# Optimization experiments

Measured on AMD Instinct MI355X. Metric: run time of the kernel, lower is better.

The kernel has to match this reference:

```python
import jax, jax.numpy as jnp
import numpy as np

DIM = 192
HEADS = 6
G = 16          # window size (ds_flag=0 dense attention)
B = 1
H_SZ = 256
W_SZ = 256
POS_DIM = 12    # (dim//4)//4
HIDDEN = 768    # 4*dim


def _ln(x, g, b, eps=1e-5):
    m = jnp.mean(x, -1, keepdims=True)
    v = jnp.var(x, -1, keepdims=True)
    return (x - m) / jnp.sqrt(v + eps) * g + b


def setup_inputs() -> dict:
    key = jax.random.key(0)
    ks = jax.random.split(key, 8)
    s = 0.05
    return {
        "x": jax.random.normal(ks[0], (B, H_SZ * W_SZ, DIM), jnp.float32),
        "gamma1": jnp.ones((DIM,), jnp.float32),
        "beta1": jnp.zeros((DIM,), jnp.float32),
        "qkv_w": jax.random.normal(ks[1], (DIM, 3 * DIM), jnp.float32) * s,
        "qkv_b": jnp.zeros((3 * DIM,), jnp.float32),
        "proj_w": jax.random.normal(ks[2], (DIM, DIM), jnp.float32) * s,
        "proj_b": jnp.zeros((DIM,), jnp.float32),
        "pos_proj_w": jax.random.normal(ks[3], (2, POS_DIM), jnp.float32) * s,
        "pos_proj_b": jnp.zeros((POS_DIM,), jnp.float32),
        "ln1_g": jnp.ones((POS_DIM,), jnp.float32),
        "ln1_b": jnp.zeros((POS_DIM,), jnp.float32),
        "pos1_w": jax.random.normal(ks[4], (POS_DIM, POS_DIM), jnp.float32) * s,
        "pos1_b": jnp.zeros((POS_DIM,), jnp.float32),
        "ln2_g": jnp.ones((POS_DIM,), jnp.float32),
        "ln2_b": jnp.zeros((POS_DIM,), jnp.float32),
        "pos2_w": jax.random.normal(ks[5], (POS_DIM, POS_DIM), jnp.float32) * s,
        "pos2_b": jnp.zeros((POS_DIM,), jnp.float32),
        "ln3_g": jnp.ones((POS_DIM,), jnp.float32),
        "ln3_b": jnp.zeros((POS_DIM,), jnp.float32),
        "pos3_w": jax.random.normal(ks[6], (POS_DIM, HEADS), jnp.float32) * s,
        "pos3_b": jnp.zeros((HEADS,), jnp.float32),
        "gamma2": jnp.ones((DIM,), jnp.float32),
        "beta2": jnp.zeros((DIM,), jnp.float32),
        "fc1_w": jax.random.normal(ks[7], (DIM, HIDDEN), jnp.float32) * s,
        "fc1_b": jnp.zeros((HIDDEN,), jnp.float32),
        "fc2_w": jax.random.normal(jax.random.fold_in(key, 9), (HIDDEN, DIM), jnp.float32) * s,
        "fc2_b": jnp.zeros((DIM,), jnp.float32),
        "H": H_SZ,
        "W": W_SZ,
    }


def reference(x, gamma1, beta1, qkv_w, qkv_b, proj_w, proj_b,
              pos_proj_w, pos_proj_b, ln1_g, ln1_b, pos1_w, pos1_b,
              ln2_g, ln2_b, pos2_w, pos2_b, ln3_g, ln3_b, pos3_w, pos3_b,
              gamma2, beta2, fc1_w, fc1_b, fc2_w, fc2_b, H, W):
    Bx, L, C = x.shape
    h = HEADS
    d = C // h
    N = G * G
    shortcut = x
    xn = _ln(x, gamma1, beta1)
    # window partition (H, W divisible by G -> no padding, attn_mask=None)
    xw = xn.reshape(Bx, H // G, G, W // G, G, C).transpose(0, 1, 3, 2, 4, 5)
    xw = xw.reshape(-1, N, C)                       # [B_, N, C]
    B_ = xw.shape[0]
    qkv = (xw @ qkv_w + qkv_b).reshape(B_, N, 3, h, d)
    q = qkv[:, :, 0].transpose(0, 2, 1, 3) * (d ** -0.5)   # [B_, h, N, d]
    k = qkv[:, :, 1].transpose(0, 2, 1, 3)
    v = qkv[:, :, 2].transpose(0, 2, 1, 3)
    attn = jnp.einsum('bhnd,bhmd->bhnm', q, k)      # [B_, h, N, N]
    # dynamic relative position bias (DynamicPosBias MLP + gather)
    r = jnp.arange(1 - G, G)
    biases = jnp.stack(jnp.meshgrid(r, r, indexing='ij')).reshape(2, -1).T.astype(x.dtype)  # [(2G-1)^2, 2]
    p = biases @ pos_proj_w + pos_proj_b
    p = jax.nn.relu(_ln(p, ln1_g, ln1_b)) @ pos1_w + pos1_b
    p = jax.nn.relu(_ln(p, ln2_g, ln2_b)) @ pos2_w + pos2_b
    p = jax.nn.relu(_ln(p, ln3_g, ln3_b)) @ pos3_w + pos3_b  # [(2G-1)^2, heads]
    c = jnp.stack(jnp.meshgrid(jnp.arange(G), jnp.arange(G), indexing='ij')).reshape(2, -1)
    rel = c[:, :, None] - c[:, None, :]             # [2, N, N]
    idx = (rel[0] + G - 1) * (2 * G - 1) + (rel[1] + G - 1)  # [N, N]
    attn = attn + p[idx].transpose(2, 0, 1)[None]   # add [1, h, N, N] bias
    attn = jax.nn.softmax(attn, axis=-1)
    out = jnp.einsum('bhnm,bhmd->bhnd', attn, v).transpose(0, 2, 1, 3).reshape(B_, N, C)
    out = out @ proj_w + proj_b
    # window reverse
    out = out.reshape(Bx, H // G, W // G, G, G, C).transpose(0, 1, 3, 2, 4, 5).reshape(Bx, L, C)
    x = shortcut + out
    y = _ln(x, gamma2, beta2)
    y = jax.nn.gelu(y @ fc1_w + fc1_b, approximate=False) @ fc2_w + fc2_b
    return x + y
```

## Files before the change

### kernel.cpp

```cpp
#include <hip/hip_runtime.h>
#include <hip/hip_bf16.h>

#define DIM 192
#define HEADS 6
#define QKV_N 576
#define HIDDEN 768
#define M_ROWS 65536

typedef unsigned short ushortT;
typedef __attribute__((ext_vector_type(8))) short short8v;
typedef __attribute__((ext_vector_type(4))) float f32x4;
typedef __attribute__((ext_vector_type(4))) unsigned int u32x4;

#define QSCALE_L2E 0.2550348649f
#define LOG2E 1.4426950408889634f

__device__ __forceinline__ float bf2f(ushortT u) {
    union { unsigned int i; float f; } c; c.i = ((unsigned int)u) << 16; return c.f;
}
__device__ __forceinline__ ushortT f2bf(float f) {
    union { float f; unsigned int i; } c; c.f = f;
    unsigned int i = c.i;
    return (ushortT)((i + 0x7fffu + ((i >> 16) & 1u)) >> 16);
}
__device__ __forceinline__ float fast_gelu(float v) {
    float x3 = v * v * v;
    float z = fmaf(x3, -0.1029537917f, v * -2.302205077f);
    float e = exp2f(z);
    return v * __builtin_amdgcn_rcpf(1.0f + e);
}

#define GLOBAL_LOAD_LDS16(gp, lp) \
    __builtin_amdgcn_global_load_lds((const __attribute__((address_space(1))) void*)(gp), \
                                     (__attribute__((address_space(3))) void*)(lp), 16, 0, 0)

__device__ __forceinline__ void ln_relu_mm12(const float* in, const float* g, const float* b,
                                             const float* w, const float* bb, float* out, int nout) {
    float m = 0.f;
#pragma unroll
    for (int j = 0; j < 12; ++j) m += in[j];
    m *= (1.0f / 12.0f);
    float v = 0.f;
#pragma unroll
    for (int j = 0; j < 12; ++j) { float d = in[j] - m; v += d * d; }
    v *= (1.0f / 12.0f);
    float r = rsqrtf(v + 1e-5f);
    float t[12];
#pragma unroll
    for (int j = 0; j < 12; ++j) t[j] = fmaxf((in[j] - m) * r * g[j] + b[j], 0.0f);
    for (int j2 = 0; j2 < nout; ++j2) {
        float s = bb[j2];
#pragma unroll
        for (int j = 0; j < 12; ++j) s = fmaf(t[j], w[j * nout + j2], s);
        out[j2] = s;
    }
}

__global__ __launch_bounds__(256) void prep_kernel(
        const float* __restrict__ qkv_w, const float* __restrict__ proj_w,
        const float* __restrict__ fc1_w, const float* __restrict__ fc2_w,
        ushortT* __restrict__ qkv_wt, ushortT* __restrict__ proj_wt,
        ushortT* __restrict__ fc1_wt, ushortT* __restrict__ fc2_wt,
        const float* __restrict__ pw, const float* __restrict__ pb,
        const float* __restrict__ g1, const float* __restrict__ b1,
        const float* __restrict__ w1, const float* __restrict__ bb1,
        const float* __restrict__ g2, const float* __restrict__ b2,
        const float* __restrict__ w2, const float* __restrict__ bb2,
        const float* __restrict__ g3, const float* __restrict__ b3,
        const float* __restrict__ w3, const float* __restrict__ bb3,
        float* __restrict__ BTf) {
    __shared__ float tile[32][33];
    int blk = blockIdx.x;
    int t = threadIdx.x;
    if (blk < 432) {
        const float* W; ushortT* Wt; int K, N, bx, by; bool perm = false;
        if (blk < 108)      { W = qkv_w;  Wt = qkv_wt;  K = 192; N = 576; bx = blk % 18;        by = blk / 18; }
        else if (blk < 144) { int r = blk - 108; W = proj_w; Wt = proj_wt; K = 192; N = 192; bx = r % 6;  by = r / 6; }
        else if (blk < 288) { int r = blk - 144; W = fc1_w;  Wt = fc1_wt;  K = 192; N = 768; bx = r % 24; by = r / 24; }
        else                { int r = blk - 288; W = fc2_w;  Wt = fc2_wt;  K = 768; N = 192; bx = r % 6;  by = r / 6; perm = true; }
        int tx = t & 31, ty = t >> 5;
        int bX = bx * 32, bY = by * 32;
#pragma unroll
        for (int i = 0; i < 32; i += 8)
            tile[ty + i][tx] = W[(size_t)(bY + ty + i) * N + bX + tx];
        __syncthreads();
        int kcol = perm ? (((tx & 15) << 1) | (tx >> 4)) : tx;
#pragma unroll
        for (int i = 0; i < 32; i += 8)
            Wt[(size_t)(bX + ty + i) * K + bY + kcol] = f2bf(tile[tx][ty + i]);
    } else {
        int blk2 = blk - 432;
        int h = blk2 >> 8, q = blk2 & 255, kv = t;
        float di = (float)((q >> 4) - (kv >> 4));
        float dj = (float)((q & 15) - (kv & 15));
        float a[12], hh[12];
#pragma unroll
        for (int j = 0; j < 12; ++j) a[j] = di * pw[j] + dj * pw[12 + j] + pb[j];
        ln_relu_mm12(a, g1, b1, w1, bb1, hh, 12);
        ln_relu_mm12(hh, g2, b2, w2, bb2, a, 12);
        float m = 0.f;
#pragma unroll
        for (int j = 0; j < 12; ++j) m += a[j];
        m *= (1.0f / 12.0f);
        float v = 0.f;
#pragma unroll
        for (int j = 0; j < 12; ++j) { float d = a[j] - m; v += d * d; }
        v *= (1.0f / 12.0f);
        float r = rsqrtf(v + 1e-5f);
        float s = bb3[h];
#pragma unroll
        for (int j = 0; j < 12; ++j)
            s = fmaf(fmaxf((a[j] - m) * r * g3[j] + b3[j], 0.0f), w3[j * 6 + h], s);
        int wid = q >> 6, mf = (q >> 4) & 3, l4 = (q >> 2) & 3, rr = q & 3;
        int kc = kv >> 5, cc = kv & 31;
        int cf = (cc >> 4) & 1, l15 = cc & 15;
        int lane = l4 * 16 + l15;
        size_t off = ((size_t)((h * 8 + kc) * 32 + wid * 8 + mf * 2 + cf)) * 256 + lane * 4 + rr;
        BTf[off] = s * LOG2E;
    }
}

__global__ __launch_bounds__(256) void ln_kernel(const float* __restrict__ x,
                                                 const float* __restrict__ g,
                                                 const float* __restrict__ b,
                                                 ushortT* __restrict__ out) {
    int lane = threadIdx.x & 63;
    size_t row = (size_t)blockIdx.x * 4 + (threadIdx.x >> 6);
    const float* xr = x + row * DIM;
    float v0 = xr[lane], v1 = xr[lane + 64], v2 = xr[lane + 128];
    float s = v0 + v1 + v2;
    float ss = v0 * v0 + v1 * v1 + v2 * v2;
#pragma unroll
    for (int off = 32; off > 0; off >>= 1) {
        s += __shfl_xor(s, off);
        ss += __shfl_xor(ss, off);
    }
    float mean = s * (1.0f / DIM);
    float rstd = rsqrtf(ss * (1.0f / DIM) - mean * mean + 1e-5f);
    ushortT* o = out + row * DIM;
    o[lane]       = f2bf((v0 - mean) * rstd * g[lane]       + b[lane]);
    o[lane + 64]  = f2bf((v1 - mean) * rstd * g[lane + 64]  + b[lane + 64]);
    o[lane + 128] = f2bf((v2 - mean) * rstd * g[lane + 128] + b[lane + 128]);
}

template <int MODE, int NY, int KK>
__global__ __launch_bounds__(256) void mfma_gemm(const ushortT* __restrict__ A,
                                                 const ushortT* __restrict__ Wt,
                                                 const float* __restrict__ bias,
                                                 const float* __restrict__ resid,
                                                 void* __restrict__ outp,
                                                 int N) {
    __shared__ ushortT As[2][128 * 64];
    __shared__ ushortT Bs[2][64 * 64];
    const int NT = KK / 64;
    int tid = threadIdx.x;
    int lane = tid & 63, wid = tid >> 6;
    int l15 = lane & 15, l4 = lane >> 4;
    int wr = wid >> 1, wc = wid & 1;
    int p = blockIdx.x;
    int cpx = gridDim.x >> 3;
    int logical = (p & 7) * cpx + (p >> 3);
    int bx = logical / NY;
    int by = logical - bx * NY;
    int bm = bx * 128, bn = by * 64;

    f32x4 acc[4][2];
#pragma unroll
    for (int mf = 0; mf < 4; ++mf)
#pragma unroll
        for (int nf = 0; nf < 2; ++nf)
#pragma unroll
            for (int r = 0; r < 4; ++r) acc[mf][nf][r] = 0.f;

    int srow = tid >> 3;
    int schunk = (tid & 7) ^ (srow & 7);
    const ushortT* agp = A + (size_t)(bm + srow) * KK + schunk * 8;
    const ushortT* bgp = Wt + (size_t)(bn + srow) * KK + schunk * 8;

    auto STAGE = [&](int buf, int t) {
        int k0 = t * 64;
#pragma unroll
        for (int i = 0; i < 4; ++i)
            GLOBAL_LOAD_LDS16(agp + (size_t)i * 32 * KK + k0, &As[buf][i * 2048 + wid * 512]);
#pragma unroll
        for (int i = 0; i < 2; ++i)
            GLOBAL_LOAD_LDS16(bgp + (size_t)i * 32 * KK + k0, &Bs[buf][i * 2048 + wid * 512]);
    };

    STAGE(0, 0);
    for (int t = 0; t < NT; ++t) {
        int cur = t & 1;
        if (t + 1 < NT) {
            STAGE(cur ^ 1, t + 1);
            asm volatile("s_waitcnt vmcnt(6)" ::: "memory");
        } else {
            asm volatile("s_waitcnt vmcnt(0)" ::: "memory");
        }
        __builtin_amdgcn_s_barrier();
        const ushortT* Asc = As[cur];
        const ushortT* Bsc = Bs[cur];
#pragma unroll
        for (int ks = 0; ks < 2; ++ks) {
            short8v af[4], bf[2];
#pragma unroll
            for (int mf = 0; mf < 4; ++mf) {
                int row = wr * 64 + mf * 16 + l15;
                af[mf] = *(const short8v*)&Asc[row * 64 + (((ks * 4 + l4) ^ (l15 & 7)) << 3)];
            }
#pragma unroll
            for (int nf = 0; nf < 2; ++nf) {
                int row = wc * 32 + nf * 16 + l15;
                bf[nf] = *(const short8v*)&Bsc[row * 64 + (((ks * 4 + l4) ^ (l15 & 7)) << 3)];
            }
#pragma unroll
            for (int mf = 0; mf < 4; ++mf)
#pragma unroll
                for (int nf = 0; nf < 2; ++nf)
                    acc[mf][nf] = __builtin_amdgcn_mfma_f32_16x16x32_bf16(af[mf], bf[nf], acc[mf][nf], 0, 0, 0);
        }
        __builtin_amdgcn_s_barrier();
    }
#pragma unroll
    for (int mf = 0; mf < 4; ++mf) {
        size_t row = (size_t)bm + wr * 64 + mf * 16 + l4 * 4;
#pragma unroll
        for (int nf = 0; nf < 2; ++nf) {
            int col = bn + wc * 32 + nf * 16 + l15;
            float bv = bias[col];
#pragma unroll
            for (int r = 0; r < 4; ++r) {
                size_t off = (row + r) * (size_t)N + col;
                float v = acc[mf][nf][r] + bv;
                if (MODE == 0) {
                    if (col < 192) v *= QSCALE_L2E;
                    ((ushortT*)outp)[off] = f2bf(v);
                } else {
                    ((float*)outp)[off] = resid[off] + v;
                }
            }
        }
    }
}

__global__ __launch_bounds__(256, 2) void mlp_kernel(float* out,
                                                     const ushortT* __restrict__ fc1t,
                                                     const ushortT* __restrict__ fc2t,
                                                     const float* __restrict__ fc1b,
                                                     const float* __restrict__ fc2b,
                                                     const float* __restrict__ g,
                                                     const float* __restrict__ b) {
    __shared__ ushortT Bs1[2][64 * 192];
    __shared__ ushortT Bs2[192 * 64];
    __shared__ unsigned int Yl[4][16 * 32];
    int tid = threadIdx.x, lane = tid & 63, wid = tid >> 6;
    int l15 = lane & 15, l4 = lane >> 4;
    size_t bm = (size_t)blockIdx.x * 64;

    int aoff1[6], aoff2[6];
#pragma unroll
    for (int i = 0; i < 6; ++i) {
        int u = tid + i * 256;
        int r1 = u / 24, rem = u - r1 * 24;
        int kt = rem >> 3, wp = rem & 7;
        aoff1[i] = r1 * 192 + kt * 64 + ((wp ^ (r1 & 7)) << 3);
        int r2 = u >> 3, wp2 = u & 7;
        aoff2[i] = r2 * 768 + ((wp2 ^ (r2 & 7)) << 3);
    }
    auto STAGE_B1 = [&](int buf, int hc) {
#pragma unroll
        for (int i = 0; i < 6; ++i)
            GLOBAL_LOAD_LDS16(fc1t + hc * 12288 + aoff1[i], &Bs1[buf][(wid * 64 + i * 256) * 8]);
    };
    auto STAGE_B2 = [&](int hc) {
#pragma unroll
        for (int i = 0; i < 6; ++i)
            GLOBAL_LOAD_LDS16(fc2t + hc * 64 + aoff2[i], &Bs2[(wid * 64 + i * 256) * 8]);
    };

    STAGE_B1(0, 0);

    short8v af[6];
    {
        int row = wid * 16 + l15;
        const float* xr = out + (bm + row) * 192;
        float v[6][8];
        float s = 0.f, ss = 0.f;
#pragma unroll
        for (int f = 0; f < 6; ++f) {
            int base = (f >> 1) * 64 + (f & 1) * 32 + l4 * 8;
            f32x4 a0 = *(const f32x4*)(xr + base);
            f32x4 a1 = *(const f32x4*)(xr + base + 4);
#pragma unroll
            for (int j = 0; j < 4; ++j) {
                v[f][j] = a0[j]; v[f][4 + j] = a1[j];
                s += a0[j] + a1[j];
                ss += a0[j] * a0[j] + a1[j] * a1[j];
            }
        }
        s += __shfl_xor(s, 16); ss += __shfl_xor(ss, 16);
        s += __shfl_xor(s, 32); ss += __shfl_xor(ss, 32);
        float mean = s * (1.0f / 192.0f);
        float rstd = rsqrtf(ss * (1.0f / 192.0f) - mean * mean + 1e-5f);
#pragma unroll
        for (int f = 0; f < 6; ++f) {
            int base = (f >> 1) * 64 + (f & 1) * 32 + l4 * 8;
#pragma unroll
            for (int j = 0; j < 8; ++j)
                af[f][j] = (short)f2bf((v[f][j] - mean) * rstd * g[base + j] + b[base + j]);
        }
    }

    f32x4 accO[12];
#pragma unroll
    for (int nf = 0; nf < 12; ++nf)
#pragma unroll
        for (int r = 0; r < 4; ++r) accO[nf][r] = 0.f;

    for (int hc = 0; hc < 12; ++hc) {
        int cur = hc & 1;
        if (hc < 11) STAGE_B1(cur ^ 1, hc + 1);
        STAGE_B2(hc);
        if (hc < 11) asm volatile("s_waitcnt vmcnt(12)" ::: "memory");
        else         asm volatile("s_waitcnt vmcnt(6)"  ::: "memory");
        __builtin_amdgcn_s_barrier();
        f32x4 ya[4];
#pragma unroll
        for (int n = 0; n < 4; ++n) {
            float bv = fc1b[hc * 64 + n * 16 + l15];
            ya[n][0] = bv; ya[n][1] = bv; ya[n][2] = bv; ya[n][3] = bv;
        }
        __builtin_amdgcn_s_setprio(1);
#pragma unroll
        for (int kt = 0; kt < 3; ++kt)
#pragma unroll
            for (int ks = 0; ks < 2; ++ks) {
                int wp = ((ks * 4 + l4) ^ (l15 & 7)) << 3;
#pragma unroll
                for (int n = 0; n < 4; ++n) {
                    short8v bf = *(const short8v*)&Bs1[cur][(n * 16 + l15) * 192 + kt * 64 + wp];
                    ya[n] = __builtin_amdgcn_mfma_f32_16x16x32_bf16(af[kt * 2 + ks], bf, ya[n], 0, 0, 0);
                }
            }
        __builtin_amdgcn_s_setprio(0);
#pragma unroll
        for (int r = 0; r < 4; ++r) {
            int row = 4 * l4 + r;
            int key = row & 7;
#pragma unroll
            for (int gg = 0; gg < 2; ++gg) {
                float y0 = fast_gelu(ya[gg * 2 + 0][r]);
                float y1 = fast_gelu(ya[gg * 2 + 1][r]);
                unsigned int pk;
                asm("v_cvt_pk_bf16_f32 %0, %1, %2" : "=v"(pk) : "v"(y0), "v"(y1));
                int ucol = gg * 16 + l15;
                int ch = (ucol >> 2) ^ key;
                Yl[wid][row * 32 + ch * 4 + (ucol & 3)] = pk;
            }
        }
        if (hc < 11) asm volatile("s_waitcnt vmcnt(6)" ::: "memory");
        else         asm volatile("s_waitcnt vmcnt(0)" ::: "memory");
        __builtin_amdgcn_s_barrier();
        __builtin_amdgcn_s_setprio(1);
#pragma unroll
        for (int gg = 0; gg < 2; ++gg) {
            u32x4 pr = *(const u32x4*)&Yl[wid][l15 * 32 + (((gg * 4 + l4) ^ (l15 & 7)) << 2)];
            short8v pa = __builtin_bit_cast(short8v, pr);
#pragma unroll
            for (int nf = 0; nf < 12; ++nf) {
                short8v bf = *(const short8v*)&Bs2[(nf * 16 + l15) * 64 + (((gg * 4 + l4) ^ (l15 & 7)) << 3)];
                accO[nf] = __builtin_amdgcn_mfma_f32_16x16x32_bf16(pa, bf, accO[nf], 0, 0, 0);
            }
        }
        __builtin_amdgcn_s_setprio(0);
        __builtin_amdgcn_s_barrier();
    }
    size_t row0 = bm + wid * 16 + l4 * 4;
#pragma unroll
    for (int nf = 0; nf < 12; ++nf) {
        int col = nf * 16 + l15;
        float bv = fc2b[col];
#pragma unroll
        for (int r = 0; r < 4; ++r) {
            size_t off = (row0 + r) * 192 + col;
            out[off] = out[off] + bv + accO[nf][r];
        }
    }
}

__global__ __launch_bounds__(256, 4) void attn_mfma_kernel(const ushortT* __restrict__ qkv,
                                                           const float* __restrict__ BTf,
                                                           ushortT* __restrict__ O) {
    __shared__ ushortT Vt[32][264];
    __shared__ unsigned int Ps[4][64][20];
    int wh = blockIdx.x;
    int w = wh / 6, h = wh - w * 6;
    int wi = w >> 4, wj = w & 15;
    int tid = threadIdx.x, lane = tid & 63, wid = tid >> 6;
    int l15 = lane & 15, l4 = lane >> 4;

    {
        int t = tid;
        int pcol = (t & ~31) | (((t & 15) << 1) | ((t >> 4) & 1));
        size_t gr = (size_t)((wi * 16 + (t >> 4)) * 256 + wj * 16 + (t & 15));
        const ushortT* vp = qkv + gr * 576 + 384 + h * 32;
#pragma unroll
        for (int d0 = 0; d0 < 32; d0 += 8) {
            short8v u = *(const short8v*)(vp + d0);
#pragma unroll
            for (int j = 0; j < 8; ++j) Vt[d0 + j][pcol] = (ushortT)u[j];
        }
    }
    short8v qf[4];
    int qbase = wid * 64;
#pragma unroll
    for (int mf = 0; mf < 4; ++mf) {
        int q = qbase + mf * 16 + l15;
        size_t gr = (size_t)((wi * 16 + (q >> 4)) * 256 + wj * 16 + (q & 15));
        qf[mf] = *(const short8v*)(qkv + gr * 576 + h * 32 + l4 * 8);
    }
    __syncthreads();

    float l_run[4][4];
    f32x4 accO[4][2];
#pragma unroll
    for (int mf = 0; mf < 4; ++mf)
#pragma unroll
        for (int r = 0; r < 4; ++r) {
            l_run[mf][r] = 0.f;
            accO[mf][0][r] = 0.f;
            accO[mf][1][r] = 0.f;
        }
    const float* btb = BTf + ((size_t)(h * 8) * 32 + wid * 8) * 256 + lane * 4;

    for (int kc = 0; kc < 8; ++kc) {
        short8v kf[2];
#pragma unroll
        for (int cf = 0; cf < 2; ++cf) {
            int kv = kc * 32 + cf * 16 + l15;
            size_t gr = (size_t)((wi * 16 + (kv >> 4)) * 256 + wj * 16 + (kv & 15));
            kf[cf] = *(const short8v*)(qkv + gr * 576 + 192 + h * 32 + l4 * 8);
        }
        short8v vb[2];
#pragma unroll
        for (int nf = 0; nf < 2; ++nf)
            vb[nf] = *(const short8v*)&Vt[nf * 16 + l15][kc * 32 + l4 * 8];
#pragma unroll
        for (int mf = 0; mf < 4; ++mf) {
            f32x4 s0 = *(const f32x4*)(btb + (size_t)(kc * 32 + mf * 2 + 0) * 256);
            f32x4 s1 = *(const f32x4*)(btb + (size_t)(kc * 32 + mf * 2 + 1) * 256);
            __builtin_amdgcn_s_setprio(1);
            s0 = __builtin_amdgcn_mfma_f32_16x16x32_bf16(qf[mf], kf[0], s0, 0, 0, 0);
            s1 = __builtin_amdgcn_mfma_f32_16x16x32_bf16(qf[mf], kf[1], s1, 0, 0, 0);
            __builtin_amdgcn_s_setprio(0);
#pragma unroll
            for (int r = 0; r < 4; ++r) {
                float p0 = exp2f(s0[r]);
                float p1 = exp2f(s1[r]);
                l_run[mf][r] += p0 + p1;
                unsigned int pk;
                asm("v_cvt_pk_bf16_f32 %0, %1, %2" : "=v"(pk) : "v"(p0), "v"(p1));
                Ps[wid][mf * 16 + 4 * l4 + r][l15] = pk;
            }
            u32x4 pr = *(const u32x4*)&Ps[wid][mf * 16 + l15][l4 * 4];
            short8v pa = __builtin_bit_cast(short8v, pr);
            __builtin_amdgcn_s_setprio(1);
            accO[mf][0] = __builtin_amdgcn_mfma_f32_16x16x32_bf16(pa, vb[0], accO[mf][0], 0, 0, 0);
            accO[mf][1] = __builtin_amdgcn_mfma_f32_16x16x32_bf16(pa, vb[1], accO[mf][1], 0, 0, 0);
            __builtin_amdgcn_s_setprio(0);
        }
    }
#pragma unroll
    for (int mf = 0; mf < 4; ++mf)
#pragma unroll
        for (int r = 0; r < 4; ++r) {
            float l = l_run[mf][r];
            l += __shfl_xor(l, 1);
            l += __shfl_xor(l, 2);
            l += __shfl_xor(l, 4);
            l += __shfl_xor(l, 8);
            l_run[mf][r] = 1.0f / l;
        }
#pragma unroll
    for (int mf = 0; mf < 4; ++mf) {
        int q0 = qbase + mf * 16 + 4 * l4;
#pragma unroll
        for (int r = 0; r < 4; ++r) {
            int q = q0 + r;
            size_t gr = (size_t)((wi * 16 + (q >> 4)) * 256 + wj * 16 + (q & 15));
            ushortT* op = O + gr * 192 + h * 32 + l15;
            float inv = l_run[mf][r];
            op[0]  = f2bf(accO[mf][0][r] * inv);
            op[16] = f2bf(accO[mf][1][r] * inv);
        }
    }
}

extern "C" void kernel_launch(void* const* d_in, const int* in_sizes, int n_in,
                              void* d_out, int out_size, void* d_ws, size_t ws_size,
                              hipStream_t stream) {
    const float* x        = (const float*)d_in[0];
    const float* gamma1   = (const float*)d_in[1];
    const float* beta1    = (const float*)d_in[2];
    const float* qkv_w    = (const float*)d_in[3];
    const float* qkv_b    = (const float*)d_in[4];
    const float* proj_w   = (const float*)d_in[5];
    const float* proj_b   = (const float*)d_in[6];
    const float* pos_proj_w = (const float*)d_in[7];
    const float* pos_proj_b = (const float*)d_in[8];
    const float* ln1_g    = (const float*)d_in[9];
    const float* ln1_b    = (const float*)d_in[10];
    const float* pos1_w   = (const float*)d_in[11];
    const float* pos1_b   = (const float*)d_in[12];
    const float* ln2_g    = (const float*)d_in[13];
    const float* ln2_b    = (const float*)d_in[14];
    const float* pos2_w   = (const float*)d_in[15];
    const float* pos2_b   = (const float*)d_in[16];
    const float* ln3_g    = (const float*)d_in[17];
    const float* ln3_b    = (const float*)d_in[18];
    const float* pos3_w   = (const float*)d_in[19];
    const float* pos3_b   = (const float*)d_in[20];
    const float* gamma2   = (const float*)d_in[21];
    const float* beta2    = (const float*)d_in[22];
    const float* fc1_w    = (const float*)d_in[23];
    const float* fc1_b    = (const float*)d_in[24];
    const float* fc2_w    = (const float*)d_in[25];
    const float* fc2_b    = (const float*)d_in[26];
    float* out = (float*)d_out;

    char* ws = (char*)d_ws;
    ushortT* qkv = (ushortT*)(ws + 0);
    ushortT* xn   = (ushortT*)(ws + 100663296);
    ushortT* Obuf = xn;
    ushortT* qkv_wt  = (ushortT*)(ws + 125829120);
    ushortT* proj_wt = (ushortT*)(ws + 126050304);
    ushortT* fc1_wt  = (ushortT*)(ws + 126124032);
    ushortT* fc2_wt  = (ushortT*)(ws + 126418944);
    float*   BTf     = (float*)(ws + 126713856);

    prep_kernel<<<1968, 256, 0, stream>>>(
        qkv_w, proj_w, fc1_w, fc2_w, qkv_wt, proj_wt, fc1_wt, fc2_wt,
        pos_proj_w, pos_proj_b, ln1_g, ln1_b, pos1_w, pos1_b,
        ln2_g, ln2_b, pos2_w, pos2_b, ln3_g, ln3_b, pos3_w, pos3_b, BTf);
    ln_kernel<<<M_ROWS / 4, 256, 0, stream>>>(x, gamma1, beta1, xn);
    mfma_gemm<0, 9, 192><<<(M_ROWS / 128) * (QKV_N / 64), 256, 0, stream>>>(
        xn, qkv_wt, qkv_b, nullptr, qkv, QKV_N);
    attn_mfma_kernel<<<1536, 256, 0, stream>>>(qkv, BTf, Obuf);
    mfma_gemm<2, 3, 192><<<(M_ROWS / 128) * (DIM / 64), 256, 0, stream>>>(
        Obuf, proj_wt, proj_b, x, out, DIM);
    mlp_kernel<<<M_ROWS / 64, 256, 0, stream>>>(
        out, fc1_wt, fc2_wt, fc1_b, fc2_b, gamma2, beta2);
}
```

Measured before the change: 206.4 us.

## Halve MLP hidden chunk to 32 and double-buffer fc2 tiles for higher occupancy

The fused MLP kernel now processes the 768-wide hidden dimension in 24 chunks of 32 instead of 12 chunks of 64. Both fc1 and fc2 weight tiles are double-buffered and staged together, and the LDS swizzles are adjusted for the narrower tiles. LDS use drops from about 88KB to about 52KB per block, and launch bounds rise to 3 blocks per CU. The goal is more latency hiding through occupancy, at the cost of twice as many barriers and loop iterations with less MFMA work per iteration.

After: 217.8 us. 1.06x slower.

```diff
diff --git a/kernel.cpp b/kernel.cpp
--- a/kernel.cpp
+++ b/kernel.cpp
@@ -242,42 +242,40 @@
     }
 }
 
-__global__ __launch_bounds__(256, 2) void mlp_kernel(float* out,
+__global__ __launch_bounds__(256, 3) void mlp_kernel(float* out,
                                                      const ushortT* __restrict__ fc1t,
                                                      const ushortT* __restrict__ fc2t,
                                                      const float* __restrict__ fc1b,
                                                      const float* __restrict__ fc2b,
                                                      const float* __restrict__ g,
                                                      const float* __restrict__ b) {
-    __shared__ ushortT Bs1[2][64 * 192];
-    __shared__ ushortT Bs2[192 * 64];
-    __shared__ unsigned int Yl[4][16 * 32];
+    __shared__ ushortT Bs1[2][32 * 192];
+    __shared__ ushortT Bs2[2][192 * 32];
+    __shared__ unsigned int Yl[4][256];
     int tid = threadIdx.x, lane = tid & 63, wid = tid >> 6;
     int l15 = lane & 15, l4 = lane >> 4;
     size_t bm = (size_t)blockIdx.x * 64;
 
-    int aoff1[6], aoff2[6];
-#pragma unroll
-    for (int i = 0; i < 6; ++i) {
+    int aoff1[3], aoff2[3];
+#pragma unroll
+    for (int i = 0; i < 3; ++i) {
         int u = tid + i * 256;
         int r1 = u / 24, rem = u - r1 * 24;
-        int kt = rem >> 3, wp = rem & 7;
-        aoff1[i] = r1 * 192 + kt * 64 + ((wp ^ (r1 & 7)) << 3);
-        int r2 = u >> 3, wp2 = u & 7;
-        aoff2[i] = r2 * 768 + ((wp2 ^ (r2 & 7)) << 3);
-    }
-    auto STAGE_B1 = [&](int buf, int hc) {
-#pragma unroll
-        for (int i = 0; i < 6; ++i)
-            GLOBAL_LOAD_LDS16(fc1t + hc * 12288 + aoff1[i], &Bs1[buf][(wid * 64 + i * 256) * 8]);
+        int kt = rem >> 3, w = rem & 7;
+        aoff1[i] = r1 * 192 + kt * 64 + ((w ^ (r1 & 7)) << 3);
+        int r2 = u >> 2, g2 = u & 3;
+        aoff2[i] = r2 * 768 + ((g2 ^ (r2 & 3)) << 3);
+    }
+    auto STAGE = [&](int buf, int hc) {
+#pragma unroll
+        for (int i = 0; i < 3; ++i)
+            GLOBAL_LOAD_LDS16(fc1t + hc * 6144 + aoff1[i], &Bs1[buf][(tid + i * 256) * 8]);
+#pragma unroll
+        for (int i = 0; i < 3; ++i)
+            GLOBAL_LOAD_LDS16(fc2t + hc * 32 + aoff2[i], &Bs2[buf][(tid + i * 256) * 8]);
     };
-    auto STAGE_B2 = [&](int hc) {
-#pragma unroll
-        for (int i = 0; i < 6; ++i)
-            GLOBAL_LOAD_LDS16(fc2t + hc * 64 + aoff2[i], &Bs2[(wid * 64 + i * 256) * 8]);
-    };
-
-    STAGE_B1(0, 0);
+
+    STAGE(0, 0);
 
     short8v af[6];
     {
@@ -316,17 +314,19 @@
 #pragma unroll
         for (int r = 0; r < 4; ++r) accO[nf][r] = 0.f;
 
-    for (int hc = 0; hc < 12; ++hc) {
+    for (int hc = 0; hc < 24; ++hc) {
         int cur = hc & 1;
-        if (hc < 11) STAGE_B1(cur ^ 1, hc + 1);
-        STAGE_B2(hc);
-        if (hc < 11) asm volatile("s_waitcnt vmcnt(12)" ::: "memory");
-        else         asm volatile("s_waitcnt vmcnt(6)"  ::: "memory");
+        if (hc < 23) {
+            STAGE(cur ^ 1, hc + 1);
+            asm volatile("s_waitcnt vmcnt(6)" ::: "memory");
+        } else {
+            asm volatile("s_waitcnt vmcnt(0)" ::: "memory");
+        }
         __builtin_amdgcn_s_barrier();
-        f32x4 ya[4];
-#pragma unroll
-        for (int n = 0; n < 4; ++n) {
-            float bv = fc1b[hc * 64 + n * 16 + l15];
+        f32x4 ya[2];
+#pragma unroll
+        for (int n = 0; n < 2; ++n) {
+            float bv = fc1b[hc * 32 + n * 16 + l15];
             ya[n][0] = bv; ya[n][1] = bv; ya[n][2] = bv; ya[n][3] = bv;
         }
         __builtin_amdgcn_s_setprio(1);
@@ -336,7 +336,7 @@
             for (int ks = 0; ks < 2; ++ks) {
                 int wp = ((ks * 4 + l4) ^ (l15 & 7)) << 3;
 #pragma unroll
-                for (int n = 0; n < 4; ++n) {
+                for (int n = 0; n < 2; ++n) {
                     short8v bf = *(const short8v*)&Bs1[cur][(n * 16 + l15) * 192 + kt * 64 + wp];
                     ya[n] = __builtin_amdgcn_mfma_f32_16x16x32_bf16(af[kt * 2 + ks], bf, ya[n], 0, 0, 0);
                 }
@@ -344,32 +344,20 @@
         __builtin_amdgcn_s_setprio(0);
 #pragma unroll
         for (int r = 0; r < 4; ++r) {
+            float y0 = fast_gelu(ya[0][r]);
+            float y1 = fast_gelu(ya[1][r]);
+            unsigned int pk;
+            asm("v_cvt_pk_bf16_f32 %0, %1, %2" : "=v"(pk) : "v"(y0), "v"(y1));
             int row = 4 * l4 + r;
-            int key = row & 7;
-#pragma unroll
-            for (int gg = 0; gg < 2; ++gg) {
-                float y0 = fast_gelu(ya[gg * 2 + 0][r]);
-                float y1 = fast_gelu(ya[gg * 2 + 1][r]);
-                unsigned int pk;
-                asm("v_cvt_pk_bf16_f32 %0, %1, %2" : "=v"(pk) : "v"(y0), "v"(y1));
-                int ucol = gg * 16 + l15;
-                int ch = (ucol >> 2) ^ key;
-                Yl[wid][row * 32 + ch * 4 + (ucol & 3)] = pk;
-            }
-        }
-        if (hc < 11) asm volatile("s_waitcnt vmcnt(6)" ::: "memory");
-        else         asm volatile("s_waitcnt vmcnt(0)" ::: "memory");
-        __builtin_amdgcn_s_barrier();
+            Yl[wid][row * 16 + ((((l15 >> 2) ^ (r & 3)) << 2) | (l15 & 3))] = pk;
+        }
+        u32x4 pr = *(const u32x4*)&Yl[wid][l15 * 16 + ((l4 ^ (l15 & 3)) << 2)];
+        short8v pa = __builtin_bit_cast(short8v, pr);
         __builtin_amdgcn_s_setprio(1);
 #pragma unroll
-        for (int gg = 0; gg < 2; ++gg) {
-            u32x4 pr = *(const u32x4*)&Yl[wid][l15 * 32 + (((gg * 4 + l4) ^ (l15 & 7)) << 2)];
-            short8v pa = __builtin_bit_cast(short8v, pr);
-#pragma unroll
-            for (int nf = 0; nf < 12; ++nf) {
-                short8v bf = *(const short8v*)&Bs2[(nf * 16 + l15) * 64 + (((gg * 4 + l4) ^ (l15 & 7)) << 3)];
-                accO[nf] = __builtin_amdgcn_mfma_f32_16x16x32_bf16(pa, bf, accO[nf], 0, 0, 0);
-            }
+        for (int nf = 0; nf < 12; ++nf) {
+            short8v bf = *(const short8v*)&Bs2[cur][(nf * 16 + l15) * 32 + ((l4 ^ (l15 & 3)) << 3)];
+            accO[nf] = __builtin_amdgcn_mfma_f32_16x16x32_bf16(pa, bf, accO[nf], 0, 0, 0);
         }
         __builtin_amdgcn_s_setprio(0);
         __builtin_amdgcn_s_barrier();
```

## Load fc2 weights directly into registers and remap attention block order

Applied to the files above, without the earlier changes.

The MLP kernel stops staging fc2 weight tiles through shared memory. Each wave now loads its fc2 fragments straight from global memory into registers. This drops the Bs2 buffer, its explicit vmcnt waits and one barrier per hidden chunk, at the cost of much higher register pressure and redundant per-wave global (L2) traffic. The attention kernel also permutes its block index so consecutive blocks are spread in groups of eight, aiming at better cache locality across XCDs.

New measurement: 302.6 us. 1.47x slower.

```diff
diff --git a/kernel.cpp b/kernel.cpp
--- a/kernel.cpp
+++ b/kernel.cpp
@@ -250,31 +250,23 @@
                                                      const float* __restrict__ g,
                                                      const float* __restrict__ b) {
     __shared__ ushortT Bs1[2][64 * 192];
-    __shared__ ushortT Bs2[192 * 64];
     __shared__ unsigned int Yl[4][16 * 32];
     int tid = threadIdx.x, lane = tid & 63, wid = tid >> 6;
     int l15 = lane & 15, l4 = lane >> 4;
     size_t bm = (size_t)blockIdx.x * 64;
 
-    int aoff1[6], aoff2[6];
+    int aoff1[6];
 #pragma unroll
     for (int i = 0; i < 6; ++i) {
         int u = tid + i * 256;
         int r1 = u / 24, rem = u - r1 * 24;
-        int kt = rem >> 3, wp = rem & 7;
-        aoff1[i] = r1 * 192 + kt * 64 + ((wp ^ (r1 & 7)) << 3);
-        int r2 = u >> 3, wp2 = u & 7;
-        aoff2[i] = r2 * 768 + ((wp2 ^ (r2 & 7)) << 3);
+        int kt = rem >> 3, w = rem & 7;
+        aoff1[i] = r1 * 192 + kt * 64 + ((w ^ (r1 & 7)) << 3);
     }
     auto STAGE_B1 = [&](int buf, int hc) {
 #pragma unroll
         for (int i = 0; i < 6; ++i)
-            GLOBAL_LOAD_LDS16(fc1t + hc * 12288 + aoff1[i], &Bs1[buf][(wid * 64 + i * 256) * 8]);
-    };
-    auto STAGE_B2 = [&](int hc) {
-#pragma unroll
-        for (int i = 0; i < 6; ++i)
-            GLOBAL_LOAD_LDS16(fc2t + hc * 64 + aoff2[i], &Bs2[(wid * 64 + i * 256) * 8]);
+            GLOBAL_LOAD_LDS16(fc1t + hc * 12288 + aoff1[i], &Bs1[buf][(tid + i * 256) * 8]);
     };
 
     STAGE_B1(0, 0);
@@ -309,6 +301,7 @@
                 af[f][j] = (short)f2bf((v[f][j] - mean) * rstd * g[base + j] + b[base + j]);
         }
     }
+    __syncthreads();
 
     f32x4 accO[12];
 #pragma unroll
@@ -319,10 +312,12 @@
     for (int hc = 0; hc < 12; ++hc) {
         int cur = hc & 1;
         if (hc < 11) STAGE_B1(cur ^ 1, hc + 1);
-        STAGE_B2(hc);
-        if (hc < 11) asm volatile("s_waitcnt vmcnt(12)" ::: "memory");
-        else         asm volatile("s_waitcnt vmcnt(6)"  ::: "memory");
-        __builtin_amdgcn_s_barrier();
+        short8v bfr[2][12];
+#pragma unroll
+        for (int gg = 0; gg < 2; ++gg)
+#pragma unroll
+            for (int nf = 0; nf < 12; ++nf)
+                bfr[gg][nf] = *(const short8v*)&fc2t[(size_t)(nf * 16 + l15) * 768 + hc * 64 + (gg * 4 + l4) * 8];
         f32x4 ya[4];
 #pragma unroll
         for (int n = 0; n < 4; ++n) {
@@ -357,19 +352,14 @@
                 Yl[wid][row * 32 + ch * 4 + (ucol & 3)] = pk;
             }
         }
-        if (hc < 11) asm volatile("s_waitcnt vmcnt(6)" ::: "memory");
-        else         asm volatile("s_waitcnt vmcnt(0)" ::: "memory");
-        __builtin_amdgcn_s_barrier();
         __builtin_amdgcn_s_setprio(1);
 #pragma unroll
         for (int gg = 0; gg < 2; ++gg) {
             u32x4 pr = *(const u32x4*)&Yl[wid][l15 * 32 + (((gg * 4 + l4) ^ (l15 & 7)) << 2)];
             short8v pa = __builtin_bit_cast(short8v, pr);
 #pragma unroll
-            for (int nf = 0; nf < 12; ++nf) {
-                short8v bf = *(const short8v*)&Bs2[(nf * 16 + l15) * 64 + (((gg * 4 + l4) ^ (l15 & 7)) << 3)];
-                accO[nf] = __builtin_amdgcn_mfma_f32_16x16x32_bf16(pa, bf, accO[nf], 0, 0, 0);
-            }
+            for (int nf = 0; nf < 12; ++nf)
+                accO[nf] = __builtin_amdgcn_mfma_f32_16x16x32_bf16(pa, bfr[gg][nf], accO[nf], 0, 0, 0);
         }
         __builtin_amdgcn_s_setprio(0);
         __builtin_amdgcn_s_barrier();
@@ -392,7 +382,8 @@
                                                            ushortT* __restrict__ O) {
     __shared__ ushortT Vt[32][264];
     __shared__ unsigned int Ps[4][64][20];
-    int wh = blockIdx.x;
+    int p = blockIdx.x;
+    int wh = (p & 7) * 192 + (p >> 3);
     int w = wh / 6, h = wh - w * 6;
     int wi = w >> 4, wj = w & 15;
     int tid = threadIdx.x, lane = tid & 63, wid = tid >> 6;
```
